# Optimization experiments

Hardware: AMD Instinct MI355X
Metric: run time of the kernel (lower is better)

## Reference

```python
import jax, jax.numpy as jnp
import numpy as np

XYZ_MIN = jnp.array([-1.0, -1.0, -1.0], dtype=jnp.float32)
XYZ_MAX = jnp.array([1.0, 1.0, 1.0], dtype=jnp.float32)
ALPHA_INIT = 0.01
ACT_SHIFT = float(np.log(1.0 / (1.0 - ALPHA_INIT) - 1.0))
INTERVAL = 0.5  # stepsize * voxel_size_ratio
NEAR, FAR = 0.2, 1.8
N_RAYS, N_SAMPLES = 4096, 256
GRID = 160
K0_DIM = 12
VIEW_PE = 4
WIDTH = 128
DIM0 = 3 + 3 * VIEW_PE * 2 + K0_DIM  # 39


def trilinear(grid, pts):
    """grid: [X,Y,Z,C]; pts: [N,3] world coords -> [N,C] (align_corners=True, border clamp)."""
    sz = jnp.array(grid.shape[:3], dtype=pts.dtype)
    ijk = (pts - XYZ_MIN) / (XYZ_MAX - XYZ_MIN) * (sz - 1.0)
    ijk = jnp.clip(ijk, 0.0, sz - 1.0)
    lo = jnp.clip(jnp.floor(ijk).astype(jnp.int32), 0, jnp.array(grid.shape[:3], jnp.int32) - 2)
    f = ijk - lo.astype(pts.dtype)
    hi = lo + 1
    x0, y0, z0 = lo[:, 0], lo[:, 1], lo[:, 2]
    x1, y1, z1 = hi[:, 0], hi[:, 1], hi[:, 2]
    fx, fy, fz = f[:, 0:1], f[:, 1:2], f[:, 2:3]
    c00 = grid[x0, y0, z0] * (1 - fz) + grid[x0, y0, z1] * fz
    c01 = grid[x0, y1, z0] * (1 - fz) + grid[x0, y1, z1] * fz
    c10 = grid[x1, y0, z0] * (1 - fz) + grid[x1, y0, z1] * fz
    c11 = grid[x1, y1, z0] * (1 - fz) + grid[x1, y1, z1] * fz
    c0 = c00 * (1 - fy) + c01 * fy
    c1 = c10 * (1 - fy) + c11 * fy
    return c0 * (1 - fx) + c1 * fx


def setup_inputs() -> dict:
    key = jax.random.key(0)
    ks = jax.random.split(key, 8)
    rays_o = jax.random.uniform(ks[0], (N_RAYS, 3), jnp.float32, -0.3, 0.3)
    rays_d = jax.random.normal(ks[1], (N_RAYS, 3), jnp.float32)
    density = jax.random.normal(ks[2], (GRID, GRID, GRID), jnp.float32)
    k0 = jax.random.normal(ks[3], (K0_DIM, GRID, GRID, GRID), jnp.float32) * 0.1
    W0 = jax.random.normal(ks[4], (DIM0, WIDTH), jnp.float32) * (1.0 / np.sqrt(DIM0))
    b0 = jnp.zeros((WIDTH,), jnp.float32)
    W1 = jax.random.normal(ks[5], (WIDTH, WIDTH), jnp.float32) * (1.0 / np.sqrt(WIDTH))
    b1 = jnp.zeros((WIDTH,), jnp.float32)
    W2 = jax.random.normal(ks[6], (WIDTH, 3), jnp.float32) * (1.0 / np.sqrt(WIDTH))
    b2 = jnp.zeros((3,), jnp.float32)
    return {"rays_o": rays_o, "rays_d": rays_d, "density": density, "k0": k0,
            "W0": W0, "b0": b0, "W1": W1, "b1": b1, "W2": W2, "b2": b2}


def reference(rays_o, rays_d, density, k0, W0, b0, W1, b1, W2, b2):
    R, S = rays_o.shape[0], N_SAMPLES
    viewdirs = rays_d / jnp.linalg.norm(rays_d, axis=-1, keepdims=True)
    t = jnp.linspace(NEAR, FAR, S, dtype=rays_o.dtype)  # [S]
    pts = rays_o[:, None, :] + rays_d[:, None, :] * t[None, :, None]  # [R,S,3]
    ptsf = pts.reshape(-1, 3)

    # Raw2Alpha: alpha = 1 - (1 + exp(d + shift))^(-interval)
    sigma = trilinear(density[..., None], ptsf)[:, 0].reshape(R, S)
    alpha = 1.0 - jnp.power(1.0 + jnp.exp(sigma + ACT_SHIFT), -INTERVAL)

    # Alphas2Weights: per-ray exclusive cumprod of transmittance
    Tcum = jnp.cumprod(1.0 - alpha + 1e-10, axis=1)  # [R,S]
    T = jnp.concatenate([jnp.ones((R, 1), alpha.dtype), Tcum[:, :-1]], axis=1)
    weights = alpha * T
    alphainv_last = Tcum[:, -1]

    # k0 features + view positional encoding -> rgbnet MLP
    feat = trilinear(jnp.moveaxis(k0, 0, -1), ptsf).reshape(R, S, K0_DIM)
    freq = (2.0 ** jnp.arange(VIEW_PE)).astype(rays_o.dtype)  # [P]
    vf = viewdirs[:, :, None] * freq[None, None, :]  # [R,3,P]
    vemb = jnp.concatenate([viewdirs, jnp.sin(vf).reshape(R, -1), jnp.cos(vf).reshape(R, -1)], axis=-1)  # [R,27]
    x = jnp.concatenate([feat, jnp.broadcast_to(vemb[:, None, :], (R, S, vemb.shape[-1]))], axis=-1)  # [R,S,39]

    h = jax.nn.relu(x @ W0 + b0)
    h = jax.nn.relu(h @ W1 + b1)
    rgb = jax.nn.sigmoid(h @ W2 + b2)  # [R,S,3]

    # composite with white background
    rgb_marched = jnp.sum(weights[..., None] * rgb, axis=1) + alphainv_last[:, None]
    return rgb_marched
```

## Files before the change

### kernel.cpp

```cpp
#include <hip/hip_runtime.h>
#include <hip/hip_bf16.h>

#define NRAYS 4096
#define NS 256
#define G 160
#define G2 (160*160)
#define G3 (160*160*160)
#define K0DIM 12
#define WIDTH 128
#define CHUNK 32
#define NCHUNK 8
#define HSTR 36
#define HBS 136
#define ACT_SHIFT_F (-4.5951198501345889f)
#define TNEAR 0.2f
#define TFAR 1.8f

typedef unsigned short u16;
typedef unsigned int u32;
typedef __attribute__((ext_vector_type(8))) short short8;
typedef __attribute__((ext_vector_type(4))) float floatx4;

#define W1F_IDX(kq, qs, n) (((((kq)<<2) + (qs)) * 128 + (n)) << 3)

__device__ __forceinline__ float bf2f(u16 u) {
    union { u32 i; float f; } v; v.i = ((u32)u) << 16; return v.f;
}
__device__ __forceinline__ u16 f2bf(float f) {
    union { float f; u32 u; } v; v.f = f;
    u32 r = v.u + 0x7FFFu + ((v.u >> 16) & 1u);
    return (u16)(r >> 16);
}

__device__ __forceinline__ float loadv(const float* p, int i) { return p[i]; }
__device__ __forceinline__ float loadv(const u16* p, int i)   { return bf2f(p[i]); }
__device__ __forceinline__ void storev(float* p, int i, float v) { p[i] = v; }
__device__ __forceinline__ void storev(u16* p, int i, float v)   { p[i] = f2bf(v); }
__device__ __forceinline__ float rawf(float x) { return x; }
__device__ __forceinline__ float rawf(u16 x)   { return bf2f(x); }

struct Coords { int idx; float fx, fy, fz; };

__device__ __forceinline__ Coords coords_for(float px, float py, float pz) {
    float gx = fminf(fmaxf((px + 1.0f) * 79.5f, 0.0f), 159.0f);
    float gy = fminf(fmaxf((py + 1.0f) * 79.5f, 0.0f), 159.0f);
    float gz = fminf(fmaxf((pz + 1.0f) * 79.5f, 0.0f), 159.0f);
    int ix = (int)gx; if (ix > 158) ix = 158;
    int iy = (int)gy; if (iy > 158) iy = 158;
    int iz = (int)gz; if (iz > 158) iz = 158;
    Coords c;
    c.idx = (ix * G + iy) * G + iz;
    c.fx = gx - (float)ix; c.fy = gy - (float)iy; c.fz = gz - (float)iz;
    return c;
}

template <typename T>
__device__ __forceinline__ float trilerp(const T* __restrict__ g, Coords c) {
    float c000 = loadv(g, c.idx);
    float c001 = loadv(g, c.idx + 1);
    float c010 = loadv(g, c.idx + G);
    float c011 = loadv(g, c.idx + G + 1);
    float c100 = loadv(g, c.idx + G2);
    float c101 = loadv(g, c.idx + G2 + 1);
    float c110 = loadv(g, c.idx + G2 + G);
    float c111 = loadv(g, c.idx + G2 + G + 1);
    float c00 = c000 * (1.0f - c.fz) + c001 * c.fz;
    float c01 = c010 * (1.0f - c.fz) + c011 * c.fz;
    float c10 = c100 * (1.0f - c.fz) + c101 * c.fz;
    float c11 = c110 * (1.0f - c.fz) + c111 * c.fz;
    float c0 = c00 * (1.0f - c.fy) + c01 * c.fy;
    float c1 = c10 * (1.0f - c.fy) + c11 * c.fy;
    return c0 * (1.0f - c.fx) + c1 * c.fx;
}

__global__ void decide_mode(const u16* __restrict__ rays_d_u16, int* __restrict__ mode) {
    if (blockIdx.x == 0 && threadIdx.x == 0) {
        int bad = 0;
        for (int i = 0; i < 128; i++) {
            u16 u = rays_d_u16[i];
            int e = (u >> 7) & 0xFF;
            int m = u & 0x7F;
            float v = bf2f(u);
            if (e == 0xFF || (e == 0 && m != 0) || fabsf(v) > 32.0f) bad++;
        }
        *mode = (bad >= 4) ? 1 : 0;
    }
}

template <typename T, typename OT, int MODE>
__global__ __launch_bounds__(256, 3)
void dvgo_fused(const T* __restrict__ rays_o, const T* __restrict__ rays_d,
                const T* __restrict__ density, const T* __restrict__ k0,
                const T* __restrict__ W0, const T* __restrict__ b0,
                const T* __restrict__ W1, const T* __restrict__ b1,
                const T* __restrict__ W2, const T* __restrict__ b2,
                OT* __restrict__ out, const int* __restrict__ mode)
{
    if (*mode != MODE) return;

    __shared__ __align__(16) u16   W1f[WIDTH * WIDTH];
    __shared__ __align__(16) u16   h0B[CHUNK * HBS];
    __shared__ __align__(16) u16   W0h[K0DIM * WIDTH];
    __shared__ __align__(16) float featT[K0DIM * HSTR];
    __shared__ __align__(16) float W2Tf[3 * WIDTH];
    __shared__ float p2[CHUNK * 6];
    __shared__ float base0[WIDTH];
    __shared__ float b1s[WIDTH];
    __shared__ float b2s[3];
    __shared__ float vembs[27];
    __shared__ float wts[NS];
    __shared__ float red[96];
    __shared__ float ainvs;

    const int r = blockIdx.x;
    const int tid = threadIdx.x;

    const float o0 = loadv(rays_o, r*3+0);
    const float o1 = loadv(rays_o, r*3+1);
    const float o2 = loadv(rays_o, r*3+2);
    const float d0 = loadv(rays_d, r*3+0);
    const float d1 = loadv(rays_d, r*3+1);
    const float d2 = loadv(rays_d, r*3+2);

    for (int idx = tid; idx < WIDTH*WIDTH; idx += 256) {
        int k = idx >> 7, n = idx & 127;
        W1f[W1F_IDX(k >> 5, (k >> 3) & 3, n) + (k & 7)] = f2bf(loadv(W1, idx));
    }
    for (int k = tid; k < K0DIM*WIDTH; k += 256) W0h[k] = f2bf(loadv(W0, k));
    for (int k = tid; k < 3*WIDTH; k += 256) {
        int c = k >> 7, i = k & 127;
        W2Tf[k] = loadv(W2, i*3 + c);
    }
    if (tid < WIDTH) b1s[tid] = loadv(b1, tid);
    if (tid < 3)     b2s[tid] = loadv(b2, tid);

    if (tid < 27) {
        float inv = rsqrtf(d0*d0 + d1*d1 + d2*d2);
        float v0 = d0*inv, v1 = d1*inv, v2 = d2*inv;
        float val;
        if (tid < 3) {
            val = (tid == 0) ? v0 : ((tid == 1) ? v1 : v2);
        } else if (tid < 15) {
            int t2 = tid - 3; int dd = t2 >> 2; int p = t2 & 3;
            float vd = (dd == 0) ? v0 : ((dd == 1) ? v1 : v2);
            val = sinf(vd * (float)(1 << p));
        } else {
            int t2 = tid - 15; int dd = t2 >> 2; int p = t2 & 3;
            float vd = (dd == 0) ? v0 : ((dd == 1) ? v1 : v2);
            val = cosf(vd * (float)(1 << p));
        }
        vembs[tid] = val;
    }
    __syncthreads();

    if (tid < WIDTH) {
        float a = loadv(b0, tid);
        #pragma unroll
        for (int i = 0; i < 27; i++)
            a += vembs[i] * loadv(W0, (K0DIM + i)*WIDTH + tid);
        base0[tid] = a;
    }

    {
        int s = tid;
        float tv = TNEAR + (TFAR - TNEAR) * ((float)s * (1.0f/(float)(NS-1)));
        Coords c = coords_for(o0 + d0*tv, o1 + d1*tv, o2 + d2*tv);
        float sigma = trilerp(density, c);
        float alpha = 1.0f - rsqrtf(1.0f + __expf(sigma + ACT_SHIFT_F));
        wts[s] = alpha;
    }
    __syncthreads();

    if (tid == 0) {
        float w = 1.0f;
        for (int s = 0; s < NS; s++) {
            float a = wts[s];
            wts[s] = a * w;
            w *= (1.0f - a + 1e-10f);
        }
        ainvs = w;
    }
    __syncthreads();

    const int jt = tid & 31;
    const int st = tid >> 5;
    const int j0 = jt * 4;
    const int s0 = st * 4;

    const int lane = tid & 63;
    const int wvid = tid >> 6;
    const int mt   = wvid & 1;
    const int nh   = wvid >> 1;
    const int q    = lane >> 4;
    const int ncol = lane & 15;
    const int arow = mt*16 + ncol;
    const int kcol = q * 8;
    const int drow0 = mt*16 + q*4;

    T    raw0[8], raw1[8];
    float fr0[3], fr1[3];
    const int ch0 = tid >> 5;
    const int sl0 = tid & 31;
    const int ch1 = 8 + (tid >> 5);
    const int sl1 = tid & 31;
    const bool has1 = (tid < 128);

    #define ISSUE_GATHER(CH, SL, C0N, RAW, FR)                                  \
        { int s_ = (C0N) + (SL);                                                \
          float tv_ = TNEAR + (TFAR - TNEAR) * ((float)s_ * (1.0f/255.0f));     \
          Coords c_ = coords_for(o0 + d0*tv_, o1 + d1*tv_, o2 + d2*tv_);        \
          const T* g_ = k0 + (size_t)(CH)*G3;                                   \
          RAW[0] = g_[c_.idx];          RAW[1] = g_[c_.idx + 1];                \
          RAW[2] = g_[c_.idx + G];      RAW[3] = g_[c_.idx + G + 1];            \
          RAW[4] = g_[c_.idx + G2];     RAW[5] = g_[c_.idx + G2 + 1];           \
          RAW[6] = g_[c_.idx + G2 + G]; RAW[7] = g_[c_.idx + G2 + G + 1];       \
          FR[0] = c_.fx; FR[1] = c_.fy; FR[2] = c_.fz; }

    #define COMMIT_GATHER(CH, SL, RAW, FR)                                      \
        { float fz_ = FR[2], fy_ = FR[1], fx_ = FR[0];                          \
          float c00_ = rawf(RAW[0])*(1.0f-fz_) + rawf(RAW[1])*fz_;              \
          float c01_ = rawf(RAW[2])*(1.0f-fz_) + rawf(RAW[3])*fz_;              \
          float c10_ = rawf(RAW[4])*(1.0f-fz_) + rawf(RAW[5])*fz_;              \
          float c11_ = rawf(RAW[6])*(1.0f-fz_) + rawf(RAW[7])*fz_;              \
          float c0_ = c00_*(1.0f-fy_) + c01_*fy_;                               \
          float c1_ = c10_*(1.0f-fy_) + c11_*fy_;                               \
          featT[(CH)*HSTR + (SL)] = c0_*(1.0f-fx_) + c1_*fx_; }

    ISSUE_GATHER(ch0, sl0, 0, raw0, fr0);
    if (has1) ISSUE_GATHER(ch1, sl1, 0, raw1, fr1);

    float rgbacc = 0.0f;

    for (int cc = 0; cc < NCHUNK; cc++) {
        const int c0 = cc * CHUNK;

        COMMIT_GATHER(ch0, sl0, raw0, fr0);
        if (has1) COMMIT_GATHER(ch1, sl1, raw1, fr1);
        __syncthreads();

        {
            float acc[4][4];
            #pragma unroll
            for (int rr = 0; rr < 4; rr++) {
                float v = base0[j0+rr];
                acc[rr][0] = v; acc[rr][1] = v; acc[rr][2] = v; acc[rr][3] = v;
            }
            #pragma unroll
            for (int i = 0; i < K0DIM; i++) {
                float4 xv = *(const float4*)&featT[i*HSTR + s0];
                ushort4 wv = *(const ushort4*)&W0h[i*WIDTH + j0];
                float w;
                w = bf2f(wv.x); acc[0][0]+=w*xv.x; acc[0][1]+=w*xv.y; acc[0][2]+=w*xv.z; acc[0][3]+=w*xv.w;
                w = bf2f(wv.y); acc[1][0]+=w*xv.x; acc[1][1]+=w*xv.y; acc[1][2]+=w*xv.z; acc[1][3]+=w*xv.w;
                w = bf2f(wv.z); acc[2][0]+=w*xv.x; acc[2][1]+=w*xv.y; acc[2][2]+=w*xv.z; acc[2][3]+=w*xv.w;
                w = bf2f(wv.w); acc[3][0]+=w*xv.x; acc[3][1]+=w*xv.y; acc[3][2]+=w*xv.z; acc[3][3]+=w*xv.w;
            }
            #pragma unroll
            for (int si = 0; si < 4; si++) {
                ushort4 h;
                h.x = f2bf(fmaxf(acc[0][si], 0.0f));
                h.y = f2bf(fmaxf(acc[1][si], 0.0f));
                h.z = f2bf(fmaxf(acc[2][si], 0.0f));
                h.w = f2bf(fmaxf(acc[3][si], 0.0f));
                *(ushort4*)&h0B[(s0+si)*HBS + j0] = h;
            }
        }
        __syncthreads();

        if (cc + 1 < NCHUNK) {
            ISSUE_GATHER(ch0, sl0, c0 + CHUNK, raw0, fr0);
            if (has1) ISSUE_GATHER(ch1, sl1, c0 + CHUNK, raw1, fr1);
        }

        {
            floatx4 acc[4];
            #pragma unroll
            for (int t = 0; t < 4; t++) {
                float bj = b1s[nh*64 + t*16 + ncol];
                acc[t] = (floatx4){bj, bj, bj, bj};
            }
            #pragma unroll
            for (int kq = 0; kq < 4; kq++) {
                short8 af = *(const short8*)&h0B[arow*HBS + kq*32 + kcol];
                #pragma unroll
                for (int t = 0; t < 4; t++) {
                    short8 bf = *(const short8*)&W1f[W1F_IDX(kq, q, nh*64 + t*16 + ncol)];
                    acc[t] = __builtin_amdgcn_mfma_f32_16x16x32_bf16(af, bf, acc[t], 0, 0, 0);
                }
            }

            float p[3][4];
            #pragma unroll
            for (int c = 0; c < 3; c++)
                { p[c][0]=0; p[c][1]=0; p[c][2]=0; p[c][3]=0; }
            #pragma unroll
            for (int t = 0; t < 4; t++) {
                int j = nh*64 + t*16 + ncol;
                float w20 = W2Tf[j], w21 = W2Tf[WIDTH + j], w22 = W2Tf[2*WIDTH + j];
                #pragma unroll
                for (int rI = 0; rI < 4; rI++) {
                    float h = fmaxf(acc[t][rI], 0.0f);
                    p[0][rI] += h * w20;
                    p[1][rI] += h * w21;
                    p[2][rI] += h * w22;
                }
            }
            #pragma unroll
            for (int m = 1; m <= 8; m <<= 1) {
                #pragma unroll
                for (int c = 0; c < 3; c++) {
                    #pragma unroll
                    for (int rI = 0; rI < 4; rI++)
                        p[c][rI] += __shfl_xor(p[c][rI], m, 64);
                }
            }
            if (ncol == 0) {
                #pragma unroll
                for (int rI = 0; rI < 4; rI++) {
                    #pragma unroll
                    for (int c = 0; c < 3; c++)
                        p2[(drow0 + rI)*6 + nh*3 + c] = p[c][rI];
                }
            }
        }
        __syncthreads();

        if (tid < 96) {
            int c = tid >> 5, s = tid & 31;
            float acc2 = b2s[c] + p2[s*6 + c] + p2[s*6 + 3 + c];
            float rgb = 1.0f / (1.0f + __expf(-acc2));
            rgbacc += wts[c0 + s] * rgb;
        }
    }

    if (tid < 96) red[tid] = rgbacc;
    __syncthreads();
    if (tid < 3) {
        float s = 0.0f;
        #pragma unroll
        for (int k = 0; k < 32; k++) s += red[tid*32 + k];
        storev(out, r*3 + tid, s + ainvs);
    }
    #undef ISSUE_GATHER
    #undef COMMIT_GATHER
}

extern "C" void kernel_launch(void* const* d_in, const int* in_sizes, int n_in,
                              void* d_out, int out_size, void* d_ws, size_t ws_size,
                              hipStream_t stream) {
    int* mode = (int*)d_ws;
    decide_mode<<<dim3(1), dim3(64), 0, stream>>>((const u16*)d_in[1], mode);

    dvgo_fused<u16, u16, 0><<<dim3(NRAYS), dim3(256), 0, stream>>>(
        (const u16*)d_in[0], (const u16*)d_in[1], (const u16*)d_in[2],
        (const u16*)d_in[3], (const u16*)d_in[4], (const u16*)d_in[5],
        (const u16*)d_in[6], (const u16*)d_in[7], (const u16*)d_in[8],
        (const u16*)d_in[9], (u16*)d_out, mode);

    dvgo_fused<float, float, 1><<<dim3(NRAYS), dim3(256), 0, stream>>>(
        (const float*)d_in[0], (const float*)d_in[1], (const float*)d_in[2],
        (const float*)d_in[3], (const float*)d_in[4], (const float*)d_in[5],
        (const float*)d_in[6], (const float*)d_in[7], (const float*)d_in[8],
        (const float*)d_in[9], (float*)d_out, mode);
}
```

Before: 545.4 us.

## Vectorize trilinear gathers with aligned z-pair loads and move layer0 to MFMA

Trilinear sampling now loads four aligned 4-element vectors, one per (x,y) corner, instead of eight scalar loads. The z-pair is picked from each vector by the in-vector offset. The first MLP layer (12 k0 features by 128) moves from scalar FMAs on a float featT tile to a bf16 MFMA, using a zero-padded 16-wide featB tile and a transposed W0 layout. This cuts gather instruction count and VALU work. In exchange, features are rounded to bf16 before layer 0, and the vector loads assume the base offset is suitably aligned (base is even, so float4 loads are only 8-byte aligned).

```diff
diff --git a/kernel.cpp b/kernel.cpp
--- a/kernel.cpp
+++ b/kernel.cpp
@@ -10,7 +10,6 @@
 #define WIDTH 128
 #define CHUNK 32
 #define NCHUNK 8
-#define HSTR 36
 #define HBS 136
 #define ACT_SHIFT_F (-4.5951198501345889f)
 #define TNEAR 0.2f
@@ -36,41 +35,36 @@
 __device__ __forceinline__ float loadv(const u16* p, int i)   { return bf2f(p[i]); }
 __device__ __forceinline__ void storev(float* p, int i, float v) { p[i] = v; }
 __device__ __forceinline__ void storev(u16* p, int i, float v)   { p[i] = f2bf(v); }
-__device__ __forceinline__ float rawf(float x) { return x; }
-__device__ __forceinline__ float rawf(u16 x)   { return bf2f(x); }
-
-struct Coords { int idx; float fx, fy, fz; };
-
-__device__ __forceinline__ Coords coords_for(float px, float py, float pz) {
+
+template <typename T> struct QT;
+template <> struct QT<u16>   { using type = ushort4; };
+template <> struct QT<float> { using type = float4;  };
+
+__device__ __forceinline__ void zpair(const ushort4& q, int d, float& v0, float& v1) {
+    u16 r0 = (d == 0) ? q.x : ((d == 1) ? q.y : q.z);
+    u16 r1 = (d == 0) ? q.y : ((d == 1) ? q.z : q.w);
+    v0 = bf2f(r0); v1 = bf2f(r1);
+}
+__device__ __forceinline__ void zpair(const float4& q, int d, float& v0, float& v1) {
+    v0 = (d == 0) ? q.x : ((d == 1) ? q.y : q.z);
+    v1 = (d == 0) ? q.y : ((d == 1) ? q.z : q.w);
+}
+
+struct CoordsE { int base; int d; float fx, fy, fz; };
+
+__device__ __forceinline__ CoordsE coords_e(float px, float py, float pz) {
     float gx = fminf(fmaxf((px + 1.0f) * 79.5f, 0.0f), 159.0f);
     float gy = fminf(fmaxf((py + 1.0f) * 79.5f, 0.0f), 159.0f);
     float gz = fminf(fmaxf((pz + 1.0f) * 79.5f, 0.0f), 159.0f);
     int ix = (int)gx; if (ix > 158) ix = 158;
     int iy = (int)gy; if (iy > 158) iy = 158;
     int iz = (int)gz; if (iz > 158) iz = 158;
-    Coords c;
-    c.idx = (ix * G + iy) * G + iz;
+    int ze = iz & ~1; if (ze > 156) ze = 156;
+    CoordsE c;
+    c.base = (ix * G + iy) * G + ze;
+    c.d = iz - ze;
     c.fx = gx - (float)ix; c.fy = gy - (float)iy; c.fz = gz - (float)iz;
     return c;
-}
-
-template <typename T>
-__device__ __forceinline__ float trilerp(const T* __restrict__ g, Coords c) {
-    float c000 = loadv(g, c.idx);
-    float c001 = loadv(g, c.idx + 1);
-    float c010 = loadv(g, c.idx + G);
-    float c011 = loadv(g, c.idx + G + 1);
-    float c100 = loadv(g, c.idx + G2);
-    float c101 = loadv(g, c.idx + G2 + 1);
-    float c110 = loadv(g, c.idx + G2 + G);
-    float c111 = loadv(g, c.idx + G2 + G + 1);
-    float c00 = c000 * (1.0f - c.fz) + c001 * c.fz;
-    float c01 = c010 * (1.0f - c.fz) + c011 * c.fz;
-    float c10 = c100 * (1.0f - c.fz) + c101 * c.fz;
-    float c11 = c110 * (1.0f - c.fz) + c111 * c.fz;
-    float c0 = c00 * (1.0f - c.fy) + c01 * c.fy;
-    float c1 = c10 * (1.0f - c.fy) + c11 * c.fy;
-    return c0 * (1.0f - c.fx) + c1 * c.fx;
 }
 
 __global__ void decide_mode(const u16* __restrict__ rays_d_u16, int* __restrict__ mode) {
@@ -98,10 +92,12 @@
 {
     if (*mode != MODE) return;
 
+    using qvec = typename QT<T>::type;
+
     __shared__ __align__(16) u16   W1f[WIDTH * WIDTH];
     __shared__ __align__(16) u16   h0B[CHUNK * HBS];
-    __shared__ __align__(16) u16   W0h[K0DIM * WIDTH];
-    __shared__ __align__(16) float featT[K0DIM * HSTR];
+    __shared__ __align__(16) u16   W0f[WIDTH * 16];
+    __shared__ __align__(16) u16   featB[CHUNK * 16];
     __shared__ __align__(16) float W2Tf[3 * WIDTH];
     __shared__ float p2[CHUNK * 6];
     __shared__ float base0[WIDTH];
@@ -126,7 +122,12 @@
         int k = idx >> 7, n = idx & 127;
         W1f[W1F_IDX(k >> 5, (k >> 3) & 3, n) + (k & 7)] = f2bf(loadv(W1, idx));
     }
-    for (int k = tid; k < K0DIM*WIDTH; k += 256) W0h[k] = f2bf(loadv(W0, k));
+    for (int i = tid; i < WIDTH*16; i += 256) {
+        int n = i >> 4, k = i & 15;
+        W0f[i] = (k < K0DIM) ? f2bf(loadv(W0, k*WIDTH + n)) : (u16)0;
+    }
+    for (int i = tid; i < CHUNK*4; i += 256)
+        featB[(i >> 2)*16 + 12 + (i & 3)] = 0;
     for (int k = tid; k < 3*WIDTH; k += 256) {
         int c = k >> 7, i = k & 127;
         W2Tf[k] = loadv(W2, i*3 + c);
@@ -164,8 +165,21 @@
     {
         int s = tid;
         float tv = TNEAR + (TFAR - TNEAR) * ((float)s * (1.0f/(float)(NS-1)));
-        Coords c = coords_for(o0 + d0*tv, o1 + d1*tv, o2 + d2*tv);
-        float sigma = trilerp(density, c);
+        CoordsE c = coords_e(o0 + d0*tv, o1 + d1*tv, o2 + d2*tv);
+        qvec q00 = *(const qvec*)(density + c.base);
+        qvec q01 = *(const qvec*)(density + c.base + G);
+        qvec q10 = *(const qvec*)(density + c.base + G2);
+        qvec q11 = *(const qvec*)(density + c.base + G2 + G);
+        float a0,a1,b0v,b1v,c0v,c1v,d0v,d1v;
+        zpair(q00, c.d, a0, a1); zpair(q01, c.d, b0v, b1v);
+        zpair(q10, c.d, c0v, c1v); zpair(q11, c.d, d0v, d1v);
+        float c00 = a0*(1.0f-c.fz) + a1*c.fz;
+        float c01 = b0v*(1.0f-c.fz) + b1v*c.fz;
+        float c10 = c0v*(1.0f-c.fz) + c1v*c.fz;
+        float c11 = d0v*(1.0f-c.fz) + d1v*c.fz;
+        float e0 = c00*(1.0f-c.fy) + c01*c.fy;
+        float e1 = c10*(1.0f-c.fy) + c11*c.fy;
+        float sigma = e0*(1.0f-c.fx) + e1*c.fx;
         float alpha = 1.0f - rsqrtf(1.0f + __expf(sigma + ACT_SHIFT_F));
         wts[s] = alpha;
     }
@@ -181,11 +195,6 @@
         ainvs = w;
     }
     __syncthreads();
-
-    const int jt = tid & 31;
-    const int st = tid >> 5;
-    const int j0 = jt * 4;
-    const int s0 = st * 4;
 
     const int lane = tid & 63;
     const int wvid = tid >> 6;
@@ -197,79 +206,82 @@
     const int kcol = q * 8;
     const int drow0 = mt*16 + q*4;
 
-    T    raw0[8], raw1[8];
-    float fr0[3], fr1[3];
+    qvec qa[4], qb[4];
+    CoordsE cea, ceb;
     const int ch0 = tid >> 5;
     const int sl0 = tid & 31;
     const int ch1 = 8 + (tid >> 5);
     const int sl1 = tid & 31;
     const bool has1 = (tid < 128);
 
-    #define ISSUE_GATHER(CH, SL, C0N, RAW, FR)                                  \
+    #define ISSUE_GATHER(CH, SL, C0N, Q, CE)                                    \
         { int s_ = (C0N) + (SL);                                                \
           float tv_ = TNEAR + (TFAR - TNEAR) * ((float)s_ * (1.0f/255.0f));     \
-          Coords c_ = coords_for(o0 + d0*tv_, o1 + d1*tv_, o2 + d2*tv_);        \
+          CE = coords_e(o0 + d0*tv_, o1 + d1*tv_, o2 + d2*tv_);                 \
           const T* g_ = k0 + (size_t)(CH)*G3;                                   \
-          RAW[0] = g_[c_.idx];          RAW[1] = g_[c_.idx + 1];                \
-          RAW[2] = g_[c_.idx + G];      RAW[3] = g_[c_.idx + G + 1];            \
-          RAW[4] = g_[c_.idx + G2];     RAW[5] = g_[c_.idx + G2 + 1];           \
-          RAW[6] = g_[c_.idx + G2 + G]; RAW[7] = g_[c_.idx + G2 + G + 1];       \
-          FR[0] = c_.fx; FR[1] = c_.fy; FR[2] = c_.fz; }
-
-    #define COMMIT_GATHER(CH, SL, RAW, FR)                                      \
-        { float fz_ = FR[2], fy_ = FR[1], fx_ = FR[0];                          \
-          float c00_ = rawf(RAW[0])*(1.0f-fz_) + rawf(RAW[1])*fz_;              \
-          float c01_ = rawf(RAW[2])*(1.0f-fz_) + rawf(RAW[3])*fz_;              \
-          float c10_ = rawf(RAW[4])*(1.0f-fz_) + rawf(RAW[5])*fz_;              \
-          float c11_ = rawf(RAW[6])*(1.0f-fz_) + rawf(RAW[7])*fz_;              \
-          float c0_ = c00_*(1.0f-fy_) + c01_*fy_;                               \
-          float c1_ = c10_*(1.0f-fy_) + c11_*fy_;                               \
-          featT[(CH)*HSTR + (SL)] = c0_*(1.0f-fx_) + c1_*fx_; }
-
-    ISSUE_GATHER(ch0, sl0, 0, raw0, fr0);
-    if (has1) ISSUE_GATHER(ch1, sl1, 0, raw1, fr1);
+          Q[0] = *(const qvec*)(g_ + CE.base);                                  \
+          Q[1] = *(const qvec*)(g_ + CE.base + G);                              \
+          Q[2] = *(const qvec*)(g_ + CE.base + G2);                             \
+          Q[3] = *(const qvec*)(g_ + CE.base + G2 + G); }
+
+    #define COMMIT_GATHER(CH, SL, Q, CE)                                        \
+        { float a0_,a1_,b0_,b1_,c0_,c1_,d0_,d1_;                                \
+          zpair(Q[0], CE.d, a0_, a1_); zpair(Q[1], CE.d, b0_, b1_);             \
+          zpair(Q[2], CE.d, c0_, c1_); zpair(Q[3], CE.d, d0_, d1_);             \
+          float fz_ = CE.fz, fy_ = CE.fy, fx_ = CE.fx;                          \
+          float c00_ = a0_*(1.0f-fz_) + a1_*fz_;                                \
+          float c01_ = b0_*(1.0f-fz_) + b1_*fz_;                                \
+          float c10_ = c0_*(1.0f-fz_) + c1_*fz_;                                \
+          float c11_ = d0_*(1.0f-fz_) + d1_*fz_;                                \
+          float e0_ = c00_*(1.0f-fy_) + c01_*fy_;                               \
+          float e1_ = c10_*(1.0f-fy_) + c11_*fy_;                               \
+          featB[(SL)*16 + (CH)] = f2bf(e0_*(1.0f-fx_) + e1_*fx_); }
+
+    ISSUE_GATHER(ch0, sl0, 0, qa, cea);
+    if (has1) ISSUE_GATHER(ch1, sl1, 0, qb, ceb);
 
     float rgbacc = 0.0f;
 
     for (int cc = 0; cc < NCHUNK; cc++) {
         const int c0 = cc * CHUNK;
 
-        COMMIT_GATHER(ch0, sl0, raw0, fr0);
-        if (has1) COMMIT_GATHER(ch1, sl1, raw1, fr1);
+        COMMIT_GATHER(ch0, sl0, qa, cea);
+        if (has1) COMMIT_GATHER(ch1, sl1, qb, ceb);
         __syncthreads();
 
         {
-            float acc[4][4];
-            #pragma unroll
-            for (int rr = 0; rr < 4; rr++) {
-                float v = base0[j0+rr];
-                acc[rr][0] = v; acc[rr][1] = v; acc[rr][2] = v; acc[rr][3] = v;
-            }
-            #pragma unroll
-            for (int i = 0; i < K0DIM; i++) {
-                float4 xv = *(const float4*)&featT[i*HSTR + s0];
-                ushort4 wv = *(const ushort4*)&W0h[i*WIDTH + j0];
-                float w;
-                w = bf2f(wv.x); acc[0][0]+=w*xv.x; acc[0][1]+=w*xv.y; acc[0][2]+=w*xv.z; acc[0][3]+=w*xv.w;
-                w = bf2f(wv.y); acc[1][0]+=w*xv.x; acc[1][1]+=w*xv.y; acc[1][2]+=w*xv.z; acc[1][3]+=w*xv.w;
-                w = bf2f(wv.z); acc[2][0]+=w*xv.x; acc[2][1]+=w*xv.y; acc[2][2]+=w*xv.z; acc[2][3]+=w*xv.w;
-                w = bf2f(wv.w); acc[3][0]+=w*xv.x; acc[3][1]+=w*xv.y; acc[3][2]+=w*xv.z; acc[3][3]+=w*xv.w;
-            }
-            #pragma unroll
-            for (int si = 0; si < 4; si++) {
-                ushort4 h;
-                h.x = f2bf(fmaxf(acc[0][si], 0.0f));
-                h.y = f2bf(fmaxf(acc[1][si], 0.0f));
-                h.z = f2bf(fmaxf(acc[2][si], 0.0f));
-                h.w = f2bf(fmaxf(acc[3][si], 0.0f));
-                *(ushort4*)&h0B[(s0+si)*HBS + j0] = h;
+            short8 af0 = {};
+            short8 bf0 = {}, bf1 = {}, bf2v = {}, bf3 = {};
+            if (q < 2) {
+                af0  = *(const short8*)&featB[arow*16 + kcol];
+                bf0  = *(const short8*)&W0f[(nh*64 +  0 + ncol)*16 + kcol];
+                bf1  = *(const short8*)&W0f[(nh*64 + 16 + ncol)*16 + kcol];
+                bf2v = *(const short8*)&W0f[(nh*64 + 32 + ncol)*16 + kcol];
+                bf3  = *(const short8*)&W0f[(nh*64 + 48 + ncol)*16 + kcol];
+            }
+            floatx4 acc0[4];
+            #pragma unroll
+            for (int t = 0; t < 4; t++) {
+                float v = base0[nh*64 + t*16 + ncol];
+                acc0[t] = (floatx4){v, v, v, v};
+            }
+            acc0[0] = __builtin_amdgcn_mfma_f32_16x16x32_bf16(af0, bf0,  acc0[0], 0, 0, 0);
+            acc0[1] = __builtin_amdgcn_mfma_f32_16x16x32_bf16(af0, bf1,  acc0[1], 0, 0, 0);
+            acc0[2] = __builtin_amdgcn_mfma_f32_16x16x32_bf16(af0, bf2v, acc0[2], 0, 0, 0);
+            acc0[3] = __builtin_amdgcn_mfma_f32_16x16x32_bf16(af0, bf3,  acc0[3], 0, 0, 0);
+            #pragma unroll
+            for (int t = 0; t < 4; t++) {
+                int j = nh*64 + t*16 + ncol;
+                #pragma unroll
+                for (int rI = 0; rI < 4; rI++)
+                    h0B[(drow0 + rI)*HBS + j] = f2bf(fmaxf(acc0[t][rI], 0.0f));
             }
         }
         __syncthreads();
 
         if (cc + 1 < NCHUNK) {
-            ISSUE_GATHER(ch0, sl0, c0 + CHUNK, raw0, fr0);
-            if (has1) ISSUE_GATHER(ch1, sl1, c0 + CHUNK, raw1, fr1);
+            ISSUE_GATHER(ch0, sl0, c0 + CHUNK, qa, cea);
+            if (has1) ISSUE_GATHER(ch1, sl1, c0 + CHUNK, qb, ceb);
         }
 
         {
```

New measurement: 522.3 us. -4.2%, faster.
